# Kernel optimization log

Measured on AMD Instinct MI355X. Metric: run time of the kernel, lower is better.

## Reference

```python
import jax, jax.numpy as jnp
import numpy as np
from itertools import product

G = 96          # voxel grid side
B = 2           # batch samples
N_PER = 60000   # occupied voxels per sample
N = B * N_PER
C_IN = 64
C_OUT = 1
NUM_BLOCKS = 2
EPS = 1e-5


def _build_kernel_map():
    """Emulate MinkowskiEngine's coordinate hash map for a k=3, stride=1, 3D conv.
    Returns batch_ids [N], and per-offset (in_idx, out_idx) padded to N with sentinel N."""
    rng = np.random.default_rng(0)
    side = G - 2  # coords in [1, G-2] so offset coords never wrap
    keys_list = []
    for b in range(B):
        lin = rng.choice(side ** 3, size=N_PER, replace=False)
        x = lin // (side * side) + 1
        y = (lin // side) % side + 1
        z = lin % side + 1
        keys_list.append(b * G ** 3 + x * G * G + y * G + z)
    keys = np.concatenate(keys_list)
    batch_ids = np.repeat(np.arange(B), N_PER).astype(np.int32)
    order = np.argsort(keys)
    skeys = keys[order]
    in_idx = np.full((27, N), N, np.int32)   # sentinel N -> zero-padded feature row
    out_idx = np.full((27, N), N, np.int32)  # sentinel N -> dropped output row
    for k, (dx, dy, dz) in enumerate(product((-1, 0, 1), repeat=3)):
        nk = keys + dx * G * G + dy * G + dz  # neighbor coordinate key per output voxel
        pos = np.searchsorted(skeys, nk)
        pc = np.clip(pos, 0, N - 1)
        valid = skeys[pc] == nk
        m = int(valid.sum())
        in_idx[k, :m] = order[pc[valid]]
        out_idx[k, :m] = np.nonzero(valid)[0]
    return batch_ids, in_idx, out_idx


def instance_norm(f, batch_ids, num_batches):
    # per-sample, per-channel normalization over all voxels of each sample (ME InstanceNorm, no affine)
    cnt = jax.ops.segment_sum(jnp.ones((f.shape[0],), f.dtype), batch_ids, num_segments=num_batches)
    mean = jax.ops.segment_sum(f, batch_ids, num_segments=num_batches) / cnt[:, None]
    fc = f - mean[batch_ids]
    var = jax.ops.segment_sum(fc * fc, batch_ids, num_segments=num_batches) / cnt[:, None]
    return fc * jax.lax.rsqrt(var + EPS)[batch_ids]


def sparse_conv(f, w, in_idx, out_idx, bias=None):
    # gather-matmul-scatter per kernel offset; w: [27, Cin, Cout]
    n = f.shape[0]
    fpad = jnp.concatenate([f, jnp.zeros((1, f.shape[1]), f.dtype)], axis=0)
    out = jnp.zeros((n + 1, w.shape[-1]), f.dtype)
    for k in range(w.shape[0]):  # static 27-iteration loop over kernel offsets
        out = out.at[out_idx[k]].add(fpad[in_idx[k]] @ w[k])
    out = out[:n]
    if bias is not None:
        out = out + bias
    return out


def setup_inputs() -> dict:
    batch_ids, in_idx, out_idx = _build_kernel_map()
    key = jax.random.key(0)
    k0, k1, k2, k3 = jax.random.split(key, 4)
    feats = jax.random.normal(k0, (N, C_IN), dtype=jnp.float32)
    w_blocks = jax.random.normal(k1, (NUM_BLOCKS, 2, 27, C_IN, C_IN), dtype=jnp.float32) * 0.02
    w_final = jax.random.normal(k2, (27, C_IN, C_OUT), dtype=jnp.float32) * 0.02
    b_final = jax.random.normal(k3, (C_OUT,), dtype=jnp.float32) * 0.02
    return {
        "feats": feats,
        "w_blocks": w_blocks,
        "w_final": w_final,
        "b_final": b_final,
        "in_idx": jnp.asarray(in_idx),
        "out_idx": jnp.asarray(out_idx),
        "batch_ids": jnp.asarray(batch_ids),
        "batch_size": B,
    }


def reference(feats, w_blocks, w_final, b_final, in_idx, out_idx, batch_ids, batch_size):
    # InstanceNorm + ReLU
    x = jax.nn.relu(instance_norm(feats, batch_ids, batch_size))
    # SparseBasicBlocks: conv -> IN -> relu -> conv -> IN -> +res -> relu
    for b in range(w_blocks.shape[0]):
        res = x
        h = sparse_conv(x, w_blocks[b, 0], in_idx, out_idx)
        h = jax.nn.relu(instance_norm(h, batch_ids, batch_size))
        h = sparse_conv(h, w_blocks[b, 1], in_idx, out_idx)
        h = instance_norm(h, batch_ids, batch_size)
        x = jax.nn.relu(h + res)
    # final conv with bias
    return sparse_conv(x, w_final, in_idx, out_idx, bias=b_final)
```

## Files before the change

kernel.cpp:

```cpp
#include <hip/hip_runtime.h>

#define NPTS 120000
#define NROW 120064
#define NB   60000
#define TAPS 27

typedef short  short8 __attribute__((ext_vector_type(8)));
typedef float  f32x4  __attribute__((ext_vector_type(4)));

__device__ __forceinline__ float bf2f(unsigned short u) {
  unsigned v = ((unsigned)u) << 16;
  float f; __builtin_memcpy(&f, &v, 4); return f;
}
__device__ __forceinline__ unsigned short f2bf(float f) {
  unsigned v; __builtin_memcpy(&v, &f, 4);
  v = v + 0x7FFFu + ((v >> 16) & 1u);
  return (unsigned short)(v >> 16);
}

__global__ __launch_bounds__(256) void k_build_nbr(const int* __restrict__ oi,
                                                   const int* __restrict__ ii,
                                                   int* __restrict__ nbr) {
  int g = blockIdx.x * 256 + threadIdx.x;
  if (g >= TAPS * NPTS) return;
  int o = oi[g];
  if (o < NPTS) nbr[(g / NPTS) * NROW + o] = ii[g];
}

__global__ __launch_bounds__(256) void k_repack(const float* __restrict__ w,
                                                unsigned short* __restrict__ wp) {
  int g = blockIdx.x * 256 + threadIdx.x;
  int e = g & 7, l = (g >> 3) & 63, f = (g >> 9) & 7, rest = g >> 12;
  int t = f >> 1, h = f & 1;
  int kk = h * 32 + (l >> 4) * 8 + e;
  int cc = t * 16 + (l & 15);
  wp[g] = f2bf(w[(rest * 64 + kk) * 64 + cc]);
}

__global__ __launch_bounds__(256) void k_stats1_f32(const float* __restrict__ F,
                                                    float* __restrict__ P) {
  int lane = threadIdx.x & 63, wave = threadIdx.x >> 6;
  int batch = blockIdx.x >> 7, bb = blockIdx.x & 127;
  const float* Fb = F + (size_t)batch * NB * 64;
  float s = 0.f, ss = 0.f;
  for (int r = bb * 4 + wave; r < NB; r += 512) {
    float v = Fb[(size_t)r * 64 + lane];
    s += v; ss += v * v;
  }
  __shared__ float ls[4][64], lss[4][64];
  ls[wave][lane] = s; lss[wave][lane] = ss;
  __syncthreads();
  if (threadIdx.x < 64) {
    float S  = ls[0][lane] + ls[1][lane] + ls[2][lane] + ls[3][lane];
    float SS = lss[0][lane] + lss[1][lane] + lss[2][lane] + lss[3][lane];
    P[blockIdx.x * 128 + lane]      = S;
    P[blockIdx.x * 128 + 64 + lane] = SS;
  }
}

__global__ __launch_bounds__(256) void k_stats1_bf(const unsigned short* __restrict__ F,
                                                   float* __restrict__ P) {
  int t = threadIdx.x;
  int cg = t & 7;
  int rg = t >> 3;
  int batch = blockIdx.x >> 7, bb = blockIdx.x & 127;
  const unsigned short* Fb = F + (size_t)batch * NB * 64;
  float s[8], ss[8];
#pragma unroll
  for (int e = 0; e < 8; ++e) { s[e] = 0.f; ss[e] = 0.f; }
  for (int r = bb * 32 + rg; r < NB; r += 128 * 32) {
    short8 v = *(const short8*)(Fb + (size_t)r * 64 + cg * 8);
#pragma unroll
    for (int e = 0; e < 8; ++e) {
      float f = bf2f((unsigned short)v[e]);
      s[e] += f; ss[e] += f * f;
    }
  }
  __shared__ float sm[2][32][64];
#pragma unroll
  for (int e = 0; e < 8; ++e) {
    sm[0][rg][cg * 8 + e] = s[e];
    sm[1][rg][cg * 8 + e] = ss[e];
  }
  __syncthreads();
  if (t < 64) {
    float S = 0.f, SS = 0.f;
#pragma unroll 8
    for (int g = 0; g < 32; ++g) { S += sm[0][g][t]; SS += sm[1][g][t]; }
    P[blockIdx.x * 128 + t]      = S;
    P[blockIdx.x * 128 + 64 + t] = SS;
  }
}

__global__ void k_stats2(const float* __restrict__ P, float* __restrict__ MRS) {
  int t = threadIdx.x;
  if (t >= 128) return;
  int b = t >> 6, c = t & 63;
  float S = 0.f, SS = 0.f;
  for (int blk = 0; blk < 128; ++blk) {
    S  += P[(b * 128 + blk) * 128 + c];
    SS += P[(b * 128 + blk) * 128 + 64 + c];
  }
  float mean = S * (1.f / NB);
  float var  = SS * (1.f / NB) - mean * mean;
  MRS[b * 128 + c]      = mean;
  MRS[b * 128 + 64 + c] = rsqrtf(var + 1e-5f);
}

__global__ __launch_bounds__(256) void k_apply_f2b(const float* __restrict__ F,
                                                   const float* __restrict__ MRS,
                                                   unsigned short* __restrict__ O) {
  int i = blockIdx.x * 256 + threadIdx.x;
  int r = i >> 3, cb = (i & 7) * 8;
  int b = (r >= NB) ? 1 : 0;
  f32x4 v0 = *((const f32x4*)F + i * 2);
  f32x4 v1 = *((const f32x4*)F + i * 2 + 1);
  short8 o;
#pragma unroll
  for (int e = 0; e < 4; ++e) {
    float f = (v0[e] - MRS[b * 128 + cb + e]) * MRS[b * 128 + 64 + cb + e];
    o[e] = (short)f2bf(fmaxf(f, 0.f));
    float g = (v1[e] - MRS[b * 128 + cb + 4 + e]) * MRS[b * 128 + 64 + cb + 4 + e];
    o[e + 4] = (short)f2bf(fmaxf(g, 0.f));
  }
  *((short8*)O + i) = o;
}

__global__ __launch_bounds__(256) void k_apply_bf(const unsigned short* __restrict__ F,
                                                  const float* __restrict__ MRS,
                                                  unsigned short* __restrict__ O) {
  int i = blockIdx.x * 256 + threadIdx.x;
  int r = i >> 3, cb = (i & 7) * 8;
  int b = (r >= NB) ? 1 : 0;
  short8 v = *((const short8*)F + i);
  short8 o;
#pragma unroll
  for (int e = 0; e < 8; ++e) {
    float f = bf2f((unsigned short)v[e]);
    f = (f - MRS[b * 128 + cb + e]) * MRS[b * 128 + 64 + cb + e];
    o[e] = (short)f2bf(fmaxf(f, 0.f));
  }
  *((short8*)O + i) = o;
}

__global__ __launch_bounds__(256) void k_apply_res_bf(const unsigned short* __restrict__ H2,
                                                      const float* __restrict__ MRS,
                                                      unsigned short* __restrict__ X) {
  int i = blockIdx.x * 256 + threadIdx.x;
  int r = i >> 3, cb = (i & 7) * 8;
  int b = (r >= NB) ? 1 : 0;
  short8 v = *((const short8*)H2 + i);
  short8 xv = *((const short8*)X + i);
  short8 o;
#pragma unroll
  for (int e = 0; e < 8; ++e) {
    float f = bf2f((unsigned short)v[e]);
    f = (f - MRS[b * 128 + cb + e]) * MRS[b * 128 + 64 + cb + e];
    f += bf2f((unsigned short)xv[e]);
    o[e] = (short)f2bf(fmaxf(f, 0.f));
  }
  *((short8*)X + i) = o;
}

__global__ __launch_bounds__(256) void k_conv64(const unsigned short* __restrict__ X,
                                                const unsigned short* __restrict__ WP,
                                                const int* __restrict__ nbr,
                                                unsigned short* __restrict__ Y) {
  const int lane = threadIdx.x & 63, wave = threadIdx.x >> 6;
  const int j0 = blockIdx.x * 256 + wave * 64;
  const int lrow = lane & 15, lk = lane >> 4;
  f32x4 acc[4][4];
#pragma unroll
  for (int g = 0; g < 4; ++g)
#pragma unroll
    for (int c = 0; c < 4; ++c) acc[g][c] = (f32x4){0.f, 0.f, 0.f, 0.f};

  for (int k = 0; k < TAPS; ++k) {
    const int* np = nbr + (size_t)k * NROW + j0 + lrow;
    int idx[4];
    idx[0] = np[0]; idx[1] = np[16]; idx[2] = np[32]; idx[3] = np[48];
    short8 a[4][2];
#pragma unroll
    for (int g = 0; g < 4; ++g) {
      a[g][0] = (short8){0,0,0,0,0,0,0,0};
      a[g][1] = (short8){0,0,0,0,0,0,0,0};
      if (idx[g] >= 0) {
        const unsigned short* rp = X + (size_t)idx[g] * 64 + lk * 8;
        a[g][0] = *(const short8*)rp;
        a[g][1] = *(const short8*)(rp + 32);
      }
    }
    const unsigned short* wpk = WP + k * 4096 + lane * 8;
#pragma unroll
    for (int ct = 0; ct < 4; ++ct) {
      short8 b0 = *(const short8*)(wpk + ct * 1024);
      short8 b1 = *(const short8*)(wpk + ct * 1024 + 512);
#pragma unroll
      for (int g = 0; g < 4; ++g) {
        acc[g][ct] = __builtin_amdgcn_mfma_f32_16x16x32_bf16(a[g][0], b0, acc[g][ct], 0, 0, 0);
        acc[g][ct] = __builtin_amdgcn_mfma_f32_16x16x32_bf16(a[g][1], b1, acc[g][ct], 0, 0, 0);
      }
    }
  }
#pragma unroll
  for (int g = 0; g < 4; ++g) {
    unsigned short* yp = Y + (size_t)(j0 + g * 16 + lk * 4) * 64 + lrow;
#pragma unroll
    for (int r = 0; r < 4; ++r) {
      yp[r * 64 +  0] = f2bf(acc[g][0][r]);
      yp[r * 64 + 16] = f2bf(acc[g][1][r]);
      yp[r * 64 + 32] = f2bf(acc[g][2][r]);
      yp[r * 64 + 48] = f2bf(acc[g][3][r]);
    }
  }
}

__global__ __launch_bounds__(256) void k_dfin(const unsigned short* __restrict__ X,
                                              const float* __restrict__ WF,
                                              float* __restrict__ D) {
  const int lane = threadIdx.x & 63, wave = threadIdx.x >> 6;
  const int j0 = blockIdx.x * 64 + wave * 16;
  const int lrow = lane & 15, lk = lane >> 4;
  const unsigned short* rp = X + (size_t)(j0 + lrow) * 64 + lk * 8;
  short8 a0 = *(const short8*)rp;
  short8 a1 = *(const short8*)(rp + 32);
  short8 b[2][2];
#pragma unroll
  for (int ct = 0; ct < 2; ++ct) {
    int col = ct * 16 + lrow;
#pragma unroll
    for (int h = 0; h < 2; ++h) {
#pragma unroll
      for (int e = 0; e < 8; ++e)
        b[ct][h][e] = (col < TAPS) ? (short)f2bf(WF[col * 64 + h * 32 + lk * 8 + e]) : (short)0;
    }
  }
  f32x4 acc0 = {0,0,0,0}, acc1 = {0,0,0,0};
  acc0 = __builtin_amdgcn_mfma_f32_16x16x32_bf16(a0, b[0][0], acc0, 0, 0, 0);
  acc0 = __builtin_amdgcn_mfma_f32_16x16x32_bf16(a1, b[0][1], acc0, 0, 0, 0);
  acc1 = __builtin_amdgcn_mfma_f32_16x16x32_bf16(a0, b[1][0], acc1, 0, 0, 0);
  acc1 = __builtin_amdgcn_mfma_f32_16x16x32_bf16(a1, b[1][1], acc1, 0, 0, 0);
  float* dp0 = D + (size_t)lrow * NROW + j0 + lk * 4;
  float* dp1 = D + (size_t)(16 + lrow) * NROW + j0 + lk * 4;
#pragma unroll
  for (int r = 0; r < 4; ++r) { dp0[r] = acc0[r]; dp1[r] = acc1[r]; }
}

__global__ __launch_bounds__(256) void k_gfin(const float* __restrict__ D,
                                              const int* __restrict__ nbr,
                                              const float* __restrict__ BF,
                                              float* __restrict__ out) {
  int j = blockIdx.x * 256 + threadIdx.x;
  if (j >= NPTS) return;
  float acc = BF[0];
#pragma unroll
  for (int k = 0; k < TAPS; ++k) {
    int idx = nbr[(size_t)k * NROW + j];
    if (idx >= 0) acc += D[(size_t)k * NROW + idx];
  }
  out[j] = acc;
}

extern "C" void kernel_launch(void* const* d_in, const int* in_sizes, int n_in,
                              void* d_out, int out_size, void* d_ws, size_t ws_size,
                              hipStream_t stream) {
  (void)in_sizes; (void)n_in; (void)out_size; (void)ws_size;
  const float* feats = (const float*)d_in[0];
  const float* wblk  = (const float*)d_in[1];
  const float* wfin  = (const float*)d_in[2];
  const float* bfin  = (const float*)d_in[3];
  const int* in_idx  = (const int*)d_in[4];
  const int* out_idx = (const int*)d_in[5];

  char* p = (char*)d_ws;
  size_t off = 0;
  auto carve = [&](size_t bytes) {
    void* r = p + off; off += (bytes + 255) & ~(size_t)255; return r;
  };
  int*            nbr = (int*)carve((size_t)TAPS * NROW * 4);
  unsigned short* Xb  = (unsigned short*)carve((size_t)NROW * 64 * 2);
  unsigned short* Hb  = (unsigned short*)carve((size_t)NROW * 64 * 2);
  unsigned short* H2b = (unsigned short*)carve((size_t)NROW * 64 * 2);
  unsigned short* WP  = (unsigned short*)carve(108u * 4096u * 2);
  float*          D   = (float*)carve((size_t)TAPS * NROW * 4);
  float*          P   = (float*)carve(256 * 128 * 4);
  float*          MRS = (float*)carve(256 * 4);

  hipMemsetAsync(nbr, 0xFF, (size_t)TAPS * NROW * 4, stream);
  k_build_nbr<<<(TAPS * NPTS + 255) / 256, 256, 0, stream>>>(out_idx, in_idx, nbr);
  k_repack<<<1728, 256, 0, stream>>>(wblk, WP);

  k_stats1_f32<<<256, 256, 0, stream>>>(feats, P);
  k_stats2<<<1, 128, 0, stream>>>(P, MRS);
  k_apply_f2b<<<3750, 256, 0, stream>>>(feats, MRS, Xb);

  k_conv64<<<NROW / 256, 256, 0, stream>>>(Xb, WP + 0 * 110592, nbr, Hb);
  k_stats1_bf<<<256, 256, 0, stream>>>(Hb, P);
  k_stats2<<<1, 128, 0, stream>>>(P, MRS);
  k_apply_bf<<<3750, 256, 0, stream>>>(Hb, MRS, Hb);
  k_conv64<<<NROW / 256, 256, 0, stream>>>(Hb, WP + 1 * 110592, nbr, H2b);
  k_stats1_bf<<<256, 256, 0, stream>>>(H2b, P);
  k_stats2<<<1, 128, 0, stream>>>(P, MRS);
  k_apply_res_bf<<<3750, 256, 0, stream>>>(H2b, MRS, Xb);

  k_conv64<<<NROW / 256, 256, 0, stream>>>(Xb, WP + 2 * 110592, nbr, Hb);
  k_stats1_bf<<<256, 256, 0, stream>>>(Hb, P);
  k_stats2<<<1, 128, 0, stream>>>(P, MRS);
  k_apply_bf<<<3750, 256, 0, stream>>>(Hb, MRS, Hb);
  k_conv64<<<NROW / 256, 256, 0, stream>>>(Hb, WP + 3 * 110592, nbr, H2b);
  k_stats1_bf<<<256, 256, 0, stream>>>(H2b, P);
  k_stats2<<<1, 128, 0, stream>>>(P, MRS);
  k_apply_res_bf<<<3750, 256, 0, stream>>>(H2b, MRS, Xb);

  k_dfin<<<NROW / 64, 256, 0, stream>>>(Xb, wfin, D);
  k_gfin<<<NROW / 256, 256, 0, stream>>>(D, nbr, bfin, (float*)d_out);
}
```

Baseline: 510.5 us.

## Fuse instance-norm statistics into sparse conv epilogue and halve rows per wave

Each conv block now computes per-batch, per-channel sums and sums of squares from the fp32 accumulators in its epilogue, reduces them through shared memory, and writes per-block partials. A single-block kernel then finishes the reduction. This removes the separate stats pass that re-read each bf16 conv output. Each wave now handles 32 rows instead of 64, giving twice as many blocks, and taps whose neighbour indices are all missing for a wave are skipped. The trade-offs are a longer serial final reduction over about 938 partials per channel and less reuse of weight loads per wave. Statistics also now come from the fp32 accumulators instead of the rounded bf16 values. The D buffer is enlarged.

```diff
diff --git a/kernel.cpp b/kernel.cpp
--- a/kernel.cpp
+++ b/kernel.cpp
@@ -4,6 +4,7 @@
 #define NROW 120064
 #define NB   60000
 #define TAPS 27
+#define NBLK (NROW / 128)
 
 typedef short  short8 __attribute__((ext_vector_type(8)));
 typedef float  f32x4  __attribute__((ext_vector_type(4)));
@@ -58,40 +59,6 @@
   }
 }
 
-__global__ __launch_bounds__(256) void k_stats1_bf(const unsigned short* __restrict__ F,
-                                                   float* __restrict__ P) {
-  int t = threadIdx.x;
-  int cg = t & 7;
-  int rg = t >> 3;
-  int batch = blockIdx.x >> 7, bb = blockIdx.x & 127;
-  const unsigned short* Fb = F + (size_t)batch * NB * 64;
-  float s[8], ss[8];
-#pragma unroll
-  for (int e = 0; e < 8; ++e) { s[e] = 0.f; ss[e] = 0.f; }
-  for (int r = bb * 32 + rg; r < NB; r += 128 * 32) {
-    short8 v = *(const short8*)(Fb + (size_t)r * 64 + cg * 8);
-#pragma unroll
-    for (int e = 0; e < 8; ++e) {
-      float f = bf2f((unsigned short)v[e]);
-      s[e] += f; ss[e] += f * f;
-    }
-  }
-  __shared__ float sm[2][32][64];
-#pragma unroll
-  for (int e = 0; e < 8; ++e) {
-    sm[0][rg][cg * 8 + e] = s[e];
-    sm[1][rg][cg * 8 + e] = ss[e];
-  }
-  __syncthreads();
-  if (t < 64) {
-    float S = 0.f, SS = 0.f;
-#pragma unroll 8
-    for (int g = 0; g < 32; ++g) { S += sm[0][g][t]; SS += sm[1][g][t]; }
-    P[blockIdx.x * 128 + t]      = S;
-    P[blockIdx.x * 128 + 64 + t] = SS;
-  }
-}
-
 __global__ void k_stats2(const float* __restrict__ P, float* __restrict__ MRS) {
   int t = threadIdx.x;
   if (t >= 128) return;
@@ -105,6 +72,22 @@
   float var  = SS * (1.f / NB) - mean * mean;
   MRS[b * 128 + c]      = mean;
   MRS[b * 128 + 64 + c] = rsqrtf(var + 1e-5f);
+}
+
+__global__ void k_stats2f(const float* __restrict__ P, float* __restrict__ MRS) {
+  int t = threadIdx.x;
+  float S = 0.f;
+  for (int blk = 0; blk < NBLK; ++blk) S += P[(size_t)blk * 256 + t];
+  __shared__ float sm[256];
+  sm[t] = S;
+  __syncthreads();
+  if (t < 128) {
+    int b = t >> 6, c = t & 63;
+    float mean = sm[(b * 2 + 0) * 64 + c] * (1.f / NB);
+    float var  = sm[(b * 2 + 1) * 64 + c] * (1.f / NB) - mean * mean;
+    MRS[b * 128 + c]      = mean;
+    MRS[b * 128 + 64 + c] = rsqrtf(var + 1e-5f);
+  }
 }
 
 __global__ __launch_bounds__(256) void k_apply_f2b(const float* __restrict__ F,
@@ -162,49 +145,48 @@
   *((short8*)X + i) = o;
 }
 
-__global__ __launch_bounds__(256) void k_conv64(const unsigned short* __restrict__ X,
-                                                const unsigned short* __restrict__ WP,
-                                                const int* __restrict__ nbr,
-                                                unsigned short* __restrict__ Y) {
+__global__ __launch_bounds__(256) void k_conv64s(const unsigned short* __restrict__ X,
+                                                 const unsigned short* __restrict__ WP,
+                                                 const int* __restrict__ nbr,
+                                                 unsigned short* __restrict__ Y,
+                                                 float* __restrict__ P) {
   const int lane = threadIdx.x & 63, wave = threadIdx.x >> 6;
-  const int j0 = blockIdx.x * 256 + wave * 64;
+  const int j0w = blockIdx.x * 128 + wave * 32;
   const int lrow = lane & 15, lk = lane >> 4;
-  f32x4 acc[4][4];
-#pragma unroll
-  for (int g = 0; g < 4; ++g)
+  f32x4 acc[2][4];
+#pragma unroll
+  for (int g = 0; g < 2; ++g)
 #pragma unroll
     for (int c = 0; c < 4; ++c) acc[g][c] = (f32x4){0.f, 0.f, 0.f, 0.f};
 
   for (int k = 0; k < TAPS; ++k) {
-    const int* np = nbr + (size_t)k * NROW + j0 + lrow;
-    int idx[4];
-    idx[0] = np[0]; idx[1] = np[16]; idx[2] = np[32]; idx[3] = np[48];
-    short8 a[4][2];
-#pragma unroll
-    for (int g = 0; g < 4; ++g) {
-      a[g][0] = (short8){0,0,0,0,0,0,0,0};
-      a[g][1] = (short8){0,0,0,0,0,0,0,0};
-      if (idx[g] >= 0) {
-        const unsigned short* rp = X + (size_t)idx[g] * 64 + lk * 8;
-        a[g][0] = *(const short8*)rp;
-        a[g][1] = *(const short8*)(rp + 32);
-      }
+    const int* np = nbr + (size_t)k * NROW + j0w + lrow;
+    int i0 = np[0], i1 = np[16];
+    if (__ballot(i0 >= 0 || i1 >= 0) == 0ull) continue;
+    short8 a00 = {0,0,0,0,0,0,0,0}, a01 = {0,0,0,0,0,0,0,0};
+    short8 a10 = {0,0,0,0,0,0,0,0}, a11 = {0,0,0,0,0,0,0,0};
+    if (i0 >= 0) {
+      const unsigned short* rp = X + (size_t)i0 * 64 + lk * 8;
+      a00 = *(const short8*)rp; a01 = *(const short8*)(rp + 32);
+    }
+    if (i1 >= 0) {
+      const unsigned short* rp = X + (size_t)i1 * 64 + lk * 8;
+      a10 = *(const short8*)rp; a11 = *(const short8*)(rp + 32);
     }
     const unsigned short* wpk = WP + k * 4096 + lane * 8;
 #pragma unroll
     for (int ct = 0; ct < 4; ++ct) {
       short8 b0 = *(const short8*)(wpk + ct * 1024);
       short8 b1 = *(const short8*)(wpk + ct * 1024 + 512);
-#pragma unroll
-      for (int g = 0; g < 4; ++g) {
-        acc[g][ct] = __builtin_amdgcn_mfma_f32_16x16x32_bf16(a[g][0], b0, acc[g][ct], 0, 0, 0);
-        acc[g][ct] = __builtin_amdgcn_mfma_f32_16x16x32_bf16(a[g][1], b1, acc[g][ct], 0, 0, 0);
-      }
-    }
-  }
-#pragma unroll
-  for (int g = 0; g < 4; ++g) {
-    unsigned short* yp = Y + (size_t)(j0 + g * 16 + lk * 4) * 64 + lrow;
+      acc[0][ct] = __builtin_amdgcn_mfma_f32_16x16x32_bf16(a00, b0, acc[0][ct], 0, 0, 0);
+      acc[0][ct] = __builtin_amdgcn_mfma_f32_16x16x32_bf16(a01, b1, acc[0][ct], 0, 0, 0);
+      acc[1][ct] = __builtin_amdgcn_mfma_f32_16x16x32_bf16(a10, b0, acc[1][ct], 0, 0, 0);
+      acc[1][ct] = __builtin_amdgcn_mfma_f32_16x16x32_bf16(a11, b1, acc[1][ct], 0, 0, 0);
+    }
+  }
+#pragma unroll
+  for (int g = 0; g < 2; ++g) {
+    unsigned short* yp = Y + (size_t)(j0w + g * 16 + lk * 4) * 64 + lrow;
 #pragma unroll
     for (int r = 0; r < 4; ++r) {
       yp[r * 64 +  0] = f2bf(acc[g][0][r]);
@@ -213,6 +195,39 @@
       yp[r * 64 + 48] = f2bf(acc[g][3][r]);
     }
   }
+  float s[4][2], q[4][2];
+#pragma unroll
+  for (int ct = 0; ct < 4; ++ct) { s[ct][0] = s[ct][1] = q[ct][0] = q[ct][1] = 0.f; }
+#pragma unroll
+  for (int g = 0; g < 2; ++g) {
+    int rowbase = j0w + g * 16 + lk * 4;
+#pragma unroll
+    for (int r = 0; r < 4; ++r) {
+      int bt = (rowbase + r) >= NB;
+#pragma unroll
+      for (int ct = 0; ct < 4; ++ct) {
+        float v = acc[g][ct][r];
+        s[ct][bt] += v; q[ct][bt] += v * v;
+      }
+    }
+  }
+  __shared__ float sred[4][4][4][64];
+#pragma unroll
+  for (int ct = 0; ct < 4; ++ct)
+#pragma unroll
+    for (int b = 0; b < 2; ++b) {
+      sred[wave][lk][b * 2 + 0][ct * 16 + lrow] = s[ct][b];
+      sred[wave][lk][b * 2 + 1][ct * 16 + lrow] = q[ct][b];
+    }
+  __syncthreads();
+  int t = threadIdx.x;
+  float S = 0.f;
+#pragma unroll
+  for (int w = 0; w < 4; ++w)
+#pragma unroll
+    for (int l2 = 0; l2 < 4; ++l2)
+      S += sred[w][l2][t >> 6][t & 63];
+  P[(size_t)blockIdx.x * 256 + t] = S;
 }
 
 __global__ __launch_bounds__(256) void k_dfin(const unsigned short* __restrict__ X,
@@ -282,8 +297,9 @@
   unsigned short* Hb  = (unsigned short*)carve((size_t)NROW * 64 * 2);
   unsigned short* H2b = (unsigned short*)carve((size_t)NROW * 64 * 2);
   unsigned short* WP  = (unsigned short*)carve(108u * 4096u * 2);
-  float*          D   = (float*)carve((size_t)TAPS * NROW * 4);
+  float*          D   = (float*)carve((size_t)32 * NROW * 4);
   float*          P   = (float*)carve(256 * 128 * 4);
+  float*          P2  = (float*)carve((size_t)NBLK * 256 * 4);
   float*          MRS = (float*)carve(256 * 4);
 
   hipMemsetAsync(nbr, 0xFF, (size_t)TAPS * NROW * 4, stream);
@@ -294,22 +310,18 @@
   k_stats2<<<1, 128, 0, stream>>>(P, MRS);
   k_apply_f2b<<<3750, 256, 0, stream>>>(feats, MRS, Xb);
 
-  k_conv64<<<NROW / 256, 256, 0, stream>>>(Xb, WP + 0 * 110592, nbr, Hb);
-  k_stats1_bf<<<256, 256, 0, stream>>>(Hb, P);
-  k_stats2<<<1, 128, 0, stream>>>(P, MRS);
+  k_conv64s<<<NBLK, 256, 0, stream>>>(Xb, WP + 0 * 110592, nbr, Hb, P2);
+  k_stats2f<<<1, 256, 0, stream>>>(P2, MRS);
   k_apply_bf<<<3750, 256, 0, stream>>>(Hb, MRS, Hb);
-  k_conv64<<<NROW / 256, 256, 0, stream>>>(Hb, WP + 1 * 110592, nbr, H2b);
-  k_stats1_bf<<<256, 256, 0, stream>>>(H2b, P);
-  k_stats2<<<1, 128, 0, stream>>>(P, MRS);
+  k_conv64s<<<NBLK, 256, 0, stream>>>(Hb, WP + 1 * 110592, nbr, H2b, P2);
+  k_stats2f<<<1, 256, 0, stream>>>(P2, MRS);
   k_apply_res_bf<<<3750, 256, 0, stream>>>(H2b, MRS, Xb);
 
-  k_conv64<<<NROW / 256, 256, 0, stream>>>(Xb, WP + 2 * 110592, nbr, Hb);
-  k_stats1_bf<<<256, 256, 0, stream>>>(Hb, P);
-  k_stats2<<<1, 128, 0, stream>>>(P, MRS);
+  k_conv64s<<<NBLK, 256, 0, stream>>>(Xb, WP + 2 * 110592, nbr, Hb, P2);
+  k_stats2f<<<1, 256, 0, stream>>>(P2, MRS);
   k_apply_bf<<<3750, 256, 0, stream>>>(Hb, MRS, Hb);
-  k_conv64<<<NROW / 256, 256, 0, stream>>>(Hb, WP + 3 * 110592, nbr, H2b);
-  k_stats1_bf<<<256, 256, 0, stream>>>(H2b, P);
-  k_stats2<<<1, 128, 0, stream>>>(P, MRS);
+  k_conv64s<<<NBLK, 256, 0, stream>>>(Hb, WP + 3 * 110592, nbr, H2b, P2);
+  k_stats2f<<<1, 256, 0, stream>>>(P2, MRS);
   k_apply_res_bf<<<3750, 256, 0, stream>>>(H2b, MRS, Xb);
 
   k_dfin<<<NROW / 64, 256, 0, stream>>>(Xb, wfin, D);
```

Result: slower. 524.5 us (+2.7%).
